# Optimization experiments

Measured on AMD Instinct MI355X. Metric: run time of the kernel, lower is better.

Reference implementation:

```python
import jax, jax.numpy as jnp
import numpy as np

B, S, H = 32, 512, 768
NHEAD, DH = 8, 96          # 8 heads * 96 = 768
E = 4096                   # edges per sample
NC = 2
NEG = -1e9
EPS = 1e-5


def _p(k, shape, scale=0.02):
    return scale * jax.random.normal(k, shape, dtype=jnp.float32)


def setup_inputs() -> dict:
    key = jax.random.key(0)
    ks = jax.random.split(key, 24)
    z = lambda *s: jnp.zeros(s, jnp.float32)
    return {
        "diff_encoded": jax.random.normal(ks[0], (B, S, H), jnp.float32),
        "msg_encoded": jax.random.normal(ks[1], (B, S, H), jnp.float32),
        "msg_mask": jnp.ones((B, S), jnp.int32),
        "edge_index_diff": jax.random.randint(ks[2], (B, 2, E), 0, S),
        "edge_index_msg": jax.random.randint(ks[3], (B, 2, E), 0, S),
        # GATv2Conv(heads=1): lin_l (source/message), lin_r (target), att vector, output bias
        "gat_wl": _p(ks[4], (H, H)), "gat_bl": z(H),
        "gat_wr": _p(ks[5], (H, H)), "gat_br": z(H),
        "gat_att": _p(ks[6], (H,)), "gat_bias": z(H),
        # cross MultiheadAttention
        "wq": _p(ks[7], (H, H)), "bq": z(H),
        "wk": _p(ks[8], (H, H)), "bk": z(H),
        "wv": _p(ks[9], (H, H)), "bv": z(H),
        "wo": _p(ks[10], (H, H)), "bo": z(H),
        # LayerNorm + MLP head
        "ln_g": jnp.ones((H,), jnp.float32), "ln_b": z(H),
        "fc0_w": _p(ks[11], (H, 512)), "fc0_b": z(512),
        "fc1_w": _p(ks[12], (512, 128)), "fc1_b": z(128),
        "fc2_w": _p(ks[13], (128, NC)), "fc2_b": z(NC),
    }


def _gat_single(x, edges, wl, bl, wr, br, att, bias):
    # GATv2Conv, heads=1, add_self_loops=True. x: [N,H], edges: [2,E] (src, dst).
    N = x.shape[0]
    src, dst = edges[0], edges[1]
    valid = (src < N) & (dst < N)            # clip_edge_index, as a mask
    src = jnp.where(valid, src, 0)
    dst = jnp.where(valid, dst, 0)
    loop = jnp.arange(N, dtype=src.dtype)    # PyG adds self loops
    src_a = jnp.concatenate([src, loop])
    dst_a = jnp.concatenate([dst, loop])
    valid_a = jnp.concatenate([valid, jnp.ones((N,), bool)])
    xl = x @ wl + bl                          # source / message transform
    xr = x @ wr + br                          # target transform
    e = jax.nn.leaky_relu(xl[src_a] + xr[dst_a], 0.2) @ att   # [E+N]
    e = jnp.where(valid_a, e, NEG)
    emax = jax.ops.segment_max(e, dst_a, num_segments=N)
    p = jnp.exp(e - emax[dst_a]) * valid_a.astype(x.dtype)
    denom = jax.ops.segment_sum(p, dst_a, num_segments=N)
    alpha = p / denom[dst_a]
    out = jax.ops.segment_sum(alpha[:, None] * xl[src_a], dst_a, num_segments=N)
    return out + bias


_gat = jax.vmap(_gat_single, in_axes=(0, 0) + (None,) * 6)


def _layernorm(x, g, b):
    mu = jnp.mean(x, -1, keepdims=True)
    var = jnp.mean(jnp.square(x - mu), -1, keepdims=True)
    return (x - mu) * jax.lax.rsqrt(var + EPS) * g + b


def reference(diff_encoded, msg_encoded, msg_mask, edge_index_diff, edge_index_msg,
              gat_wl, gat_bl, gat_wr, gat_br, gat_att, gat_bias,
              wq, bq, wk, bk, wv, bv, wo, bo, ln_g, ln_b,
              fc0_w, fc0_b, fc1_w, fc1_b, fc2_w, fc2_b):
    diff_g = _gat(diff_encoded, edge_index_diff, gat_wl, gat_bl, gat_wr, gat_br, gat_att, gat_bias) + diff_encoded
    msg_g = _gat(msg_encoded, edge_index_msg, gat_wl, gat_bl, gat_wr, gat_br, gat_att, gat_bias) + msg_encoded
    # cross attention: query=diff_g, key/value=msg_g, key_padding_mask = (msg_mask == 0)
    q = (diff_g @ wq + bq).reshape(B, S, NHEAD, DH)
    k = (msg_g @ wk + bk).reshape(B, S, NHEAD, DH)
    v = (msg_g @ wv + bv).reshape(B, S, NHEAD, DH)
    scores = jnp.einsum("bqhd,bkhd->bhqk", q, k) / jnp.sqrt(jnp.float32(DH))
    scores = jnp.where((msg_mask == 0)[:, None, None, :], NEG, scores)
    attn = jax.nn.softmax(scores, axis=-1)
    ctx = jnp.einsum("bhqk,bkhd->bqhd", attn, v).reshape(B, S, H) @ wo + bo
    fused = _layernorm(ctx + diff_g, ln_g, ln_b)
    x = fused[:, 0, :]                                  # CLS token
    x = jax.nn.relu(x @ fc0_w + fc0_b)                  # dropout = identity (eval)
    x = jax.nn.relu(x @ fc1_w + fc1_b)
    return x @ fc2_w + fc2_b
```

## Files before the change

kernel.cpp:

```cpp
#include <hip/hip_runtime.h>
#include <hip/hip_bf16.h>
#include <math.h>

#define BB 32
#define SS 512
#define HH 768
#define NHEADC 8
#define DHC 96
#define EE 4096
#define NCC 2
#define CAPC 128
#define CAP2 32
#define GSL 36
#define XRS 1536
#define NEGV -1000000000.0f
#define EPSV 1e-5f

typedef __hip_bfloat16 bf16;
typedef __bf16 bf16x8 __attribute__((ext_vector_type(8)));
typedef float f32x4 __attribute__((ext_vector_type(4)));

static __device__ inline unsigned short f2bf_u(float f) {
  __hip_bfloat16 h = __float2bfloat16(f);
  return *(unsigned short*)&h;
}
static __device__ inline float bfu(unsigned short u) {
  return __uint_as_float(((unsigned int)u) << 16);
}
static __device__ inline float bf2f(bf16 h) { return __bfloat162float(h); }

static __device__ inline void gload16(const void* g, void* l) {
  __builtin_amdgcn_global_load_lds(
      (const __attribute__((address_space(1))) void*)g,
      (__attribute__((address_space(3))) void*)l, 16, 0, 0);
}

__global__ __launch_bounds__(256) void k_cvt_bf16(const float* __restrict__ x,
                                                  bf16* __restrict__ y, int n) {
  int i = (blockIdx.x * 256 + threadIdx.x) * 4;
  if (i >= n) return;
  float4 v = *(const float4*)(x + i);
  ushort4 o;
  o.x = f2bf_u(v.x); o.y = f2bf_u(v.y); o.z = f2bf_u(v.z); o.w = f2bf_u(v.w);
  *(ushort4*)((unsigned short*)y + i) = o;
}

__global__ __launch_bounds__(256) void k_cvt_wt(
    const float* __restrict__ w0, const float* __restrict__ w1,
    const float* __restrict__ w2, const float* __restrict__ w3,
    bf16* __restrict__ o0, bf16* __restrict__ o1,
    bf16* __restrict__ o2, bf16* __restrict__ o3) {
  const float* w; bf16* o;
  switch (blockIdx.z) {
    case 0: w = w0; o = o0; break;
    case 1: w = w1; o = o1; break;
    case 2: w = w2; o = o2; break;
    default: w = w3; o = o3; break;
  }
  __shared__ float t[32][33];
  int n0 = blockIdx.x * 32, k0 = blockIdx.y * 32;
  int x = threadIdx.x & 31, y = threadIdx.x >> 5;
  for (int yy = y; yy < 32; yy += 8)
    t[yy][x] = w[(size_t)(k0 + yy) * HH + n0 + x];
  __syncthreads();
  for (int yy = y; yy < 32; yy += 8)
    o[(size_t)(n0 + yy) * HH + k0 + x] = __float2bfloat16(t[x][yy]);
}

__global__ __launch_bounds__(256) void k_bias_stack(
    const float* __restrict__ bl, const float* __restrict__ br,
    const float* __restrict__ bk, const float* __restrict__ bv,
    float* __restrict__ biasA, float* __restrict__ biasB) {
  int t = blockIdx.x * 256 + threadIdx.x;
  if (t < HH) {
    biasA[t] = bl[t]; biasA[HH + t] = br[t];
    biasB[t] = bk[t]; biasB[HH + t] = bv[t];
  }
}

template <typename OT>
__global__ __launch_bounds__(256) void k_gemm(
    const bf16* __restrict__ A, const bf16* __restrict__ Bt,
    const float* __restrict__ bias, OT* __restrict__ C,
    int M, int N, int K, int ldc)
{
  __shared__ __align__(16) bf16 As[128 * 32];
  __shared__ __align__(16) bf16 Bs[128 * 32];
  const int tid = threadIdx.x;
  const int wv = tid >> 6, lane = tid & 63;
  const int bm = blockIdx.x * 128, bn = blockIdx.y * 128;
  const int wm = (wv & 1) * 64, wn = (wv >> 1) * 64;
  const int m16 = lane & 15, half = lane >> 4;
  f32x4 acc[4][4];
  #pragma unroll
  for (int i = 0; i < 4; ++i)
    #pragma unroll
    for (int j = 0; j < 4; ++j) acc[i][j] = (f32x4){0.f, 0.f, 0.f, 0.f};

  const int c0 = tid, c1 = tid + 256;
  const int r0 = c0 >> 2, o0 = (c0 & 3) * 8;
  const int r1 = c1 >> 2, o1 = (c1 & 3) * 8;
  const size_t aB0 = (size_t)(bm + r0) * K + o0;
  const size_t aB1 = (size_t)(bm + r1) * K + o1;
  const size_t bB0 = (size_t)(bn + r0) * K + o0;
  const size_t bB1 = (size_t)(bn + r1) * K + o1;

  for (int k0 = 0; k0 < K; k0 += 32) {
    __syncthreads();
    gload16(A + aB0 + k0, As + (size_t)c0 * 8);
    gload16(A + aB1 + k0, As + (size_t)c1 * 8);
    gload16(Bt + bB0 + k0, Bs + (size_t)c0 * 8);
    gload16(Bt + bB1 + k0, Bs + (size_t)c1 * 8);
    __syncthreads();
    bf16x8 af[4], bfv[4];
    #pragma unroll
    for (int t = 0; t < 4; ++t) {
      af[t]  = *(const bf16x8*)(As + (wm + t * 16 + m16) * 32 + half * 8);
      bfv[t] = *(const bf16x8*)(Bs + (wn + t * 16 + m16) * 32 + half * 8);
    }
    #pragma unroll
    for (int i = 0; i < 4; ++i)
      #pragma unroll
      for (int j = 0; j < 4; ++j)
        acc[i][j] = __builtin_amdgcn_mfma_f32_16x16x32_bf16(af[i], bfv[j], acc[i][j], 0, 0, 0);
  }
  #pragma unroll
  for (int i = 0; i < 4; ++i) {
    #pragma unroll
    for (int j = 0; j < 4; ++j) {
      int col = bn + wn + j * 16 + m16;
      float bv = bias ? bias[col] : 0.f;
      #pragma unroll
      for (int r = 0; r < 4; ++r) {
        int row = bm + wm + i * 16 + half * 4 + r;
        float v = acc[i][j][r] + bv;
        if constexpr (sizeof(OT) == 2)
          C[(size_t)row * ldc + col] = (OT)__float2bfloat16(v);
        else
          C[(size_t)row * ldc + col] = v;
      }
    }
  }
}

__global__ __launch_bounds__(256) void k_count2(
    const int* __restrict__ e_msg, const int* __restrict__ e_diff,
    int* __restrict__ cnt, int* __restrict__ dcnt, int* __restrict__ dsrc)
{
  int i = blockIdx.x * blockDim.x + threadIdx.x;
  if (i >= BB * EE) return;
  int b = i / EE, j = i - b * EE;
  int s = e_msg[b * 2 * EE + j], d = e_msg[b * 2 * EE + EE + j];
  if (s >= 0 && s < SS && d >= 0 && d < SS)
    atomicAdd(&cnt[b * SS + d], 1);
  int s2 = e_diff[b * 2 * EE + j], d2 = e_diff[b * 2 * EE + EE + j];
  if (s2 >= 0 && s2 < SS && d2 == 0) {
    int pos = atomicAdd(&dcnt[b], 1);
    if (pos < CAPC) dsrc[b * CAPC + pos] = s2;
  }
  if (j == 0) {
    int pos = atomicAdd(&dcnt[b], 1);
    if (pos < CAPC) dsrc[b * CAPC + pos] = 0;
  }
}

__global__ __launch_bounds__(512) void k_scan(const int* __restrict__ cnt,
                                              int* __restrict__ offs,
                                              int* __restrict__ cursor) {
  __shared__ int tmp[SS];
  int b = blockIdx.x, t = threadIdx.x;
  int x = cnt[b * SS + t];
  tmp[t] = x;
  __syncthreads();
  for (int off = 1; off < SS; off <<= 1) {
    int u = (t >= off) ? tmp[t - off] : 0;
    __syncthreads();
    tmp[t] += u;
    __syncthreads();
  }
  int ex = tmp[t] - x;
  offs[b * SS + t] = ex;
  cursor[b * SS + t] = ex;
}

__global__ void k_scatter(const int* __restrict__ e_msg, int* __restrict__ cursor,
                          int* __restrict__ binned) {
  int i = blockIdx.x * blockDim.x + threadIdx.x;
  if (i >= BB * EE) return;
  int b = i / EE, j = i - b * EE;
  int s = e_msg[b * 2 * EE + j], d = e_msg[b * 2 * EE + EE + j];
  if (s >= 0 && s < SS && d >= 0 && d < SS) {
    int pos = atomicAdd(&cursor[b * SS + d], 1);
    binned[(size_t)b * EE + pos] = s;
  }
}

__global__ __launch_bounds__(256) void k_gat_fused(
    const int* __restrict__ binned, const int* __restrict__ offs,
    const int* __restrict__ cnt, const bf16* __restrict__ xlr,
    const float* __restrict__ att, const float* __restrict__ gbias,
    const float* __restrict__ resid, bf16* __restrict__ out)
{
  int g = blockIdx.x * 4 + (threadIdx.x >> 6);
  int lane = threadIdx.x & 63;
  int b = g / SS, d = g - b * SS;
  int base = offs[b * SS + d], n = cnt[b * SS + d];
  const int* bin = binned + (size_t)b * EE + base;
  float av[12];
  {
    const float4* a4 = (const float4*)att;
    #pragma unroll
    for (int r = 0; r < 3; ++r) {
      float4 t = a4[lane + 64 * r];
      av[4*r] = t.x; av[4*r+1] = t.y; av[4*r+2] = t.z; av[4*r+3] = t.w;
    }
  }
  float xr[12];
  {
    const ushort4* p = (const ushort4*)(xlr + ((size_t)b * SS + d) * XRS + HH);
    #pragma unroll
    for (int r = 0; r < 3; ++r) {
      ushort4 v = p[lane + 64 * r];
      xr[4*r] = bfu(v.x); xr[4*r+1] = bfu(v.y); xr[4*r+2] = bfu(v.z); xr[4*r+3] = bfu(v.w);
    }
  }
  float m = -3.0e38f, l = 0.f;
  float acc[12] = {};
  for (int i = -1; i < n; ++i) {
    int s = (i < 0) ? d : bin[i];
    float xs[12];
    const ushort4* p = (const ushort4*)(xlr + ((size_t)b * SS + s) * XRS);
    #pragma unroll
    for (int r = 0; r < 3; ++r) {
      ushort4 v = p[lane + 64 * r];
      xs[4*r] = bfu(v.x); xs[4*r+1] = bfu(v.y); xs[4*r+2] = bfu(v.z); xs[4*r+3] = bfu(v.w);
    }
    float e = 0.f;
    #pragma unroll
    for (int k = 0; k < 12; ++k) {
      float t = xs[k] + xr[k];
      t = t > 0.f ? t : 0.2f * t;
      e += t * av[k];
    }
    #pragma unroll
    for (int off = 32; off > 0; off >>= 1) e += __shfl_xor(e, off);
    float mn = fmaxf(m, e);
    float so = __expf(m - mn);
    float w  = __expf(e - mn);
    l = l * so + w;
    #pragma unroll
    for (int k = 0; k < 12; ++k) acc[k] = acc[k] * so + w * xs[k];
    m = mn;
  }
  float inv = 1.f / l;
  size_t o = ((size_t)b * SS + d) * HH;
  const float4* gb4 = (const float4*)gbias;
  const float4* rs4 = (const float4*)(resid + o);
  ushort4* out4 = (ushort4*)(out + o);
  #pragma unroll
  for (int r = 0; r < 3; ++r) {
    int c = lane + 64 * r;
    float4 gg = gb4[c], rr = rs4[c];
    ushort4 ov;
    ov.x = f2bf_u(acc[4*r+0] * inv + gg.x + rr.x);
    ov.y = f2bf_u(acc[4*r+1] * inv + gg.y + rr.y);
    ov.z = f2bf_u(acc[4*r+2] * inv + gg.z + rr.z);
    ov.w = f2bf_u(acc[4*r+3] * inv + gg.w + rr.w);
    out4[c] = ov;
  }
}

__global__ __launch_bounds__(192) void k_gather_diff(
    const int* __restrict__ dcnt, const int* __restrict__ dsrc,
    const float* __restrict__ diff_enc, bf16* __restrict__ G)
{
  int b = blockIdx.y, jj = blockIdx.x;
  int n = min(dcnt[b], CAP2);
  int t = threadIdx.x;
  size_t orow = ((size_t)b * GSL + jj) * HH;
  ushort4 o = {0, 0, 0, 0};
  if (jj < n || jj == CAP2) {
    int s = (jj == CAP2) ? 0 : dsrc[b * CAPC + jj];
    float4 v = ((const float4*)(diff_enc + ((size_t)b * SS + s) * HH))[t];
    o.x = f2bf_u(v.x); o.y = f2bf_u(v.y); o.z = f2bf_u(v.z); o.w = f2bf_u(v.w);
  }
  *(ushort4*)((unsigned short*)G + orow + t * 4) = o;
}

__global__ __launch_bounds__(256) void k_diff_gat0(
    const int* __restrict__ dcnt, const float* __restrict__ GD,
    const float* __restrict__ att, const float* __restrict__ gbias,
    const float* __restrict__ diff_enc, float* __restrict__ dg0)
{
  int b = blockIdx.x;
  int n = min(dcnt[b], CAP2);
  __shared__ float ee[CAP2];
  __shared__ float al[CAP2];
  __shared__ float xr0s[HH];
  int wave = threadIdx.x >> 6, lane = threadIdx.x & 63;
  for (int h = threadIdx.x; h < HH; h += 256)
    xr0s[h] = GD[((size_t)b * GSL + CAP2) * XRS + HH + h];
  __syncthreads();
  for (int jj = wave; jj < n; jj += 4) {
    const float* px = GD + ((size_t)b * GSL + jj) * XRS;
    float part = 0.f;
    #pragma unroll
    for (int r = 0; r < HH / 64; ++r) {
      int h = lane + 64 * r;
      float t = px[h] + xr0s[h];
      t = t > 0.f ? t : 0.2f * t;
      part += t * att[h];
    }
    #pragma unroll
    for (int off = 32; off > 0; off >>= 1) part += __shfl_xor(part, off);
    if (lane == 0) ee[jj] = part;
  }
  __syncthreads();
  if (threadIdx.x == 0) {
    float m = -3.0e38f;
    for (int i = 0; i < n; ++i) m = fmaxf(m, ee[i]);
    float ssum = 0.f;
    for (int i = 0; i < n; ++i) ssum += expf(ee[i] - m);
    float inv = 1.f / ssum;
    for (int i = 0; i < n; ++i) al[i] = expf(ee[i] - m) * inv;
  }
  __syncthreads();
  for (int h = threadIdx.x; h < HH; h += 256) {
    float acc = 0.f;
    for (int i = 0; i < n; ++i) acc += al[i] * GD[((size_t)b * GSL + i) * XRS + h];
    dg0[b * HH + h] = acc + gbias[h] + diff_enc[(size_t)b * SS * HH + h];
  }
}

__global__ __launch_bounds__(256) void k_colmat(
    const float* __restrict__ in, const float* __restrict__ w,
    const float* __restrict__ bias, const float* __restrict__ extra,
    float* __restrict__ outp, int Kd, int Nd, long in_stride, int relu)
{
  int b = blockIdx.y, n0 = blockIdx.x * 64;
  int tid = threadIdx.x, wv = tid >> 6, lane = tid & 63;
  __shared__ float xs[HH];
  __shared__ float red[4][64];
  const float* src = in + (size_t)b * in_stride;
  for (int k = tid; k < Kd; k += 256) xs[k] = src[k];
  __syncthreads();
  int h = n0 + lane;
  int kpw = Kd >> 2;
  int kb = wv * kpw;
  float acc = 0.f;
  for (int k = 0; k < kpw; k += 8) {
    #pragma unroll
    for (int u = 0; u < 8; ++u) {
      int kk = kb + k + u;
      acc += xs[kk] * w[(size_t)kk * Nd + h];
    }
  }
  red[wv][lane] = acc;
  __syncthreads();
  if (tid < 64) {
    float s = red[0][tid] + red[1][tid] + red[2][tid] + red[3][tid] + bias[n0 + tid];
    if (extra) s += extra[(size_t)b * Nd + n0 + tid];
    if (relu) s = fmaxf(s, 0.f);
    outp[(size_t)b * Nd + n0 + tid] = s;
  }
}

__global__ __launch_bounds__(256) void k_ln(
    const float* __restrict__ xin, const float* __restrict__ g,
    const float* __restrict__ bta, float* __restrict__ yout)
{
  int b = blockIdx.x, tid = threadIdx.x;
  __shared__ float red[4], redq[4];
  float v0 = xin[b * HH + tid];
  float v1 = xin[b * HH + tid + 256];
  float v2 = xin[b * HH + tid + 512];
  float sum = v0 + v1 + v2;
  float sq = v0 * v0 + v1 * v1 + v2 * v2;
  #pragma unroll
  for (int off = 32; off > 0; off >>= 1) { sum += __shfl_xor(sum, off); sq += __shfl_xor(sq, off); }
  int wv = tid >> 6, lane = tid & 63;
  if (lane == 0) { red[wv] = sum; redq[wv] = sq; }
  __syncthreads();
  sum = red[0] + red[1] + red[2] + red[3];
  sq = redq[0] + redq[1] + redq[2] + redq[3];
  float mu = sum / HH;
  float var = sq / HH - mu * mu;
  float scl = rsqrtf(var + EPSV);
  yout[b * HH + tid]       = (v0 - mu) * scl * g[tid]       + bta[tid];
  yout[b * HH + tid + 256] = (v1 - mu) * scl * g[tid + 256] + bta[tid + 256];
  yout[b * HH + tid + 512] = (v2 - mu) * scl * g[tid + 512] + bta[tid + 512];
}

__global__ __launch_bounds__(256) void k_fc12(
    const float* __restrict__ a0g, const float* __restrict__ fc1w,
    const float* __restrict__ fc1b, const float* __restrict__ fc2w,
    const float* __restrict__ fc2b, float* __restrict__ out)
{
  int b = blockIdx.x, tid = threadIdx.x;
  __shared__ float a0s[512];
  __shared__ float a1s[128];
  __shared__ float r1[2][128];
  for (int k = tid; k < 512; k += 256) a0s[k] = a0g[b * 512 + k];
  __syncthreads();
  int o = tid & 127, hf = tid >> 7;
  int kb = hf * 256;
  float acc = 0.f;
  for (int k = 0; k < 256; k += 8) {
    #pragma unroll
    for (int u = 0; u < 8; ++u) {
      int kk = kb + k + u;
      acc += a0s[kk] * fc1w[(size_t)kk * 128 + o];
    }
  }
  r1[hf][o] = acc;
  __syncthreads();
  if (tid < 128) a1s[tid] = fmaxf(r1[0][tid] + r1[1][tid] + fc1b[tid], 0.f);
  __syncthreads();
  if (tid < 128) {
    int oo = tid >> 6, l = tid & 63;
    float p = a1s[l] * fc2w[l * 2 + oo] + a1s[l + 64] * fc2w[(l + 64) * 2 + oo];
    #pragma unroll
    for (int off = 32; off > 0; off >>= 1) p += __shfl_xor(p, off);
    if (l == 0) out[b * NCC + oo] = p + fc2b[oo];
  }
}

__global__ __launch_bounds__(512) void k_attn(
    const float* __restrict__ q0, const bf16* __restrict__ kvb,
    const int* __restrict__ mask, float* __restrict__ ctx)
{
  int b = blockIdx.x / NHEADC, hd = blockIdx.x % NHEADC;
  __shared__ float qs[DHC];
  __shared__ float sc[SS];
  __shared__ float redm[8];
  __shared__ float reds[8];
  __shared__ float pr4[4][DHC];
  int tid = threadIdx.x;
  if (tid < DHC) qs[tid] = q0[b * HH + hd * DHC + tid];
  __syncthreads();
  const float scale = 0.10206207261596575f;
  {
    int s = tid;
    const int4* pk4 = (const int4*)(kvb + ((size_t)b * SS + s) * XRS + hd * DHC);
    float acc = 0.f;
    #pragma unroll
    for (int c = 0; c < 12; ++c) {
      int4 raw = pk4[c];
      const unsigned short* u = (const unsigned short*)&raw;
      #pragma unroll
      for (int j = 0; j < 8; ++j) acc += qs[c * 8 + j] * bfu(u[j]);
    }
    sc[s] = (mask[b * SS + s] != 0) ? acc * scale : NEGV;
  }
  __syncthreads();
  int wave = tid >> 6, lane = tid & 63;
  float m = sc[tid];
  #pragma unroll
  for (int off = 32; off > 0; off >>= 1) m = fmaxf(m, __shfl_xor(m, off));
  if (lane == 0) redm[wave] = m;
  __syncthreads();
  m = redm[0];
  #pragma unroll
  for (int i = 1; i < 8; ++i) m = fmaxf(m, redm[i]);
  float p0 = expf(sc[tid] - m);
  float ssum = p0;
  #pragma unroll
  for (int off = 32; off > 0; off >>= 1) ssum += __shfl_xor(ssum, off);
  if (lane == 0) reds[wave] = ssum;
  __syncthreads();
  ssum = reds[0] + reds[1] + reds[2] + reds[3] + reds[4] + reds[5] + reds[6] + reds[7];
  float inv = 1.f / ssum;
  sc[tid] = p0 * inv;
  __syncthreads();
  {
    int hs = tid >> 7, d = tid & 127;
    if (d < DHC) {
      const bf16* pv = kvb + ((size_t)b * SS + hs * 128) * XRS + HH + hd * DHC + d;
      float acc = 0.f;
      for (int s = 0; s < 128; s += 8) {
        #pragma unroll
        for (int u = 0; u < 8; ++u)
          acc += sc[hs * 128 + s + u] * bf2f(pv[(size_t)(s + u) * XRS]);
      }
      pr4[hs][d] = acc;
    }
  }
  __syncthreads();
  if (tid < DHC)
    ctx[b * HH + hd * DHC + tid] = pr4[0][tid] + pr4[1][tid] + pr4[2][tid] + pr4[3][tid];
}

extern "C" void kernel_launch(void* const* d_in, const int* in_sizes, int n_in,
                              void* d_out, int out_size, void* d_ws, size_t ws_size,
                              hipStream_t stream) {
  const float* diff_enc = (const float*)d_in[0];
  const float* msg_enc  = (const float*)d_in[1];
  const int*   msg_mask = (const int*)d_in[2];
  const int*   e_diff   = (const int*)d_in[3];
  const int*   e_msg    = (const int*)d_in[4];
  const float* gat_wl   = (const float*)d_in[5];
  const float* gat_bl   = (const float*)d_in[6];
  const float* gat_wr   = (const float*)d_in[7];
  const float* gat_br   = (const float*)d_in[8];
  const float* gat_att  = (const float*)d_in[9];
  const float* gat_bias = (const float*)d_in[10];
  const float* wq = (const float*)d_in[11];
  const float* bq = (const float*)d_in[12];
  const float* wk = (const float*)d_in[13];
  const float* bk = (const float*)d_in[14];
  const float* wv = (const float*)d_in[15];
  const float* bv = (const float*)d_in[16];
  const float* wo = (const float*)d_in[17];
  const float* bo = (const float*)d_in[18];
  const float* ln_g = (const float*)d_in[19];
  const float* ln_b = (const float*)d_in[20];
  const float* fc0w = (const float*)d_in[21];
  const float* fc0b = (const float*)d_in[22];
  const float* fc1w = (const float*)d_in[23];
  const float* fc1b = (const float*)d_in[24];
  const float* fc2w = (const float*)d_in[25];
  const float* fc2b = (const float*)d_in[26];
  float* out = (float*)d_out;

  char* ws = (char*)d_ws;
  size_t off = 0;
  auto alloc = [&](size_t bytes) -> void* {
    void* p = (void*)(ws + off);
    off += (bytes + 255) & ~(size_t)255;
    return p;
  };
  bf16* Abf    = (bf16*)alloc((size_t)BB * SS * HH * 2);
  bf16* xlr    = (bf16*)alloc((size_t)BB * SS * XRS * 2);
  bf16* kv     = (bf16*)alloc((size_t)BB * SS * XRS * 2);
  bf16* mg     = (bf16*)alloc((size_t)BB * SS * HH * 2);
  bf16* wtA    = (bf16*)alloc((size_t)2 * HH * HH * 2);
  bf16* wtB    = (bf16*)alloc((size_t)2 * HH * HH * 2);
  float* biasA = (float*)alloc((size_t)XRS * 4);
  float* biasB = (float*)alloc((size_t)XRS * 4);
  int*   cnt   = (int*)alloc((size_t)BB * SS * 4);
  int*   offs  = (int*)alloc((size_t)BB * SS * 4);
  int*   cursor= (int*)alloc((size_t)BB * SS * 4);
  int*   binned= (int*)alloc((size_t)BB * EE * 4);
  bf16*  G     = (bf16*)alloc((size_t)BB * GSL * HH * 2);
  float* GD    = (float*)alloc((size_t)BB * GSL * XRS * 4);
  int*   dcnt  = (int*)alloc((size_t)BB * 4);
  int*   dsrc  = (int*)alloc((size_t)BB * CAPC * 4);
  float* dg0   = (float*)alloc((size_t)BB * HH * 4);
  float* q0    = (float*)alloc((size_t)BB * HH * 4);
  float* ctx   = (float*)alloc((size_t)BB * HH * 4);
  float* fpre  = (float*)alloc((size_t)BB * HH * 4);
  float* fnrm  = (float*)alloc((size_t)BB * HH * 4);
  float* a0g   = (float*)alloc((size_t)BB * 512 * 4);

  hipMemsetAsync(cnt, 0, (size_t)BB * SS * 4, stream);
  hipMemsetAsync(dcnt, 0, (size_t)BB * 4, stream);

  const int nA = BB * SS * HH;
  k_cvt_bf16<<<nA / 1024, 256, 0, stream>>>(msg_enc, Abf, nA);
  dim3 wtGrid(HH / 32, HH / 32, 4);
  k_cvt_wt<<<wtGrid, 256, 0, stream>>>(gat_wl, gat_wr, wk, wv,
                                       wtA, wtA + (size_t)HH * HH,
                                       wtB, wtB + (size_t)HH * HH);
  k_bias_stack<<<3, 256, 0, stream>>>(gat_bl, gat_br, bk, bv, biasA, biasB);

  k_count2<<<(BB * EE + 255) / 256, 256, 0, stream>>>(e_msg, e_diff, cnt, dcnt, dsrc);
  k_scan<<<BB, SS, 0, stream>>>(cnt, offs, cursor);
  k_scatter<<<(BB * EE + 255) / 256, 256, 0, stream>>>(e_msg, cursor, binned);

  dim3 gBlk(256), gGridA((BB * SS) / 128, XRS / 128);
  k_gemm<bf16><<<gGridA, gBlk, 0, stream>>>(Abf, wtA, biasA, xlr,
                                            BB * SS, XRS, HH, XRS);
  k_gat_fused<<<(BB * SS) / 4, 256, 0, stream>>>(binned, offs, cnt, xlr,
                                                 gat_att, gat_bias, msg_enc, mg);
  k_gemm<bf16><<<gGridA, gBlk, 0, stream>>>(mg, wtB, biasB, kv,
                                            BB * SS, XRS, HH, XRS);
  {
    dim3 gg(GSL, BB);
    k_gather_diff<<<gg, 192, 0, stream>>>(dcnt, dsrc, diff_enc, G);
    dim3 gGridD((BB * GSL) / 128, XRS / 128);
    k_gemm<float><<<gGridD, gBlk, 0, stream>>>(G, wtA, biasA, GD,
                                               BB * GSL, XRS, HH, XRS);
  }
  k_diff_gat0<<<BB, 256, 0, stream>>>(dcnt, GD, gat_att, gat_bias, diff_enc, dg0);
  {
    dim3 g(HH / 64, BB);
    k_colmat<<<g, 256, 0, stream>>>(dg0, wq, bq, nullptr, q0, HH, HH, HH, 0);
  }
  k_attn<<<BB * NHEADC, 512, 0, stream>>>(q0, kv, msg_mask, ctx);
  {
    dim3 g(HH / 64, BB);
    k_colmat<<<g, 256, 0, stream>>>(ctx, wo, bo, dg0, fpre, HH, HH, HH, 0);
  }
  k_ln<<<BB, 256, 0, stream>>>(fpre, ln_g, ln_b, fnrm);
  {
    dim3 g(512 / 64, BB);
    k_colmat<<<g, 256, 0, stream>>>(fnrm, fc0w, fc0b, nullptr, a0g, HH, 512, HH, 1);
  }
  k_fc12<<<BB, 256, 0, stream>>>(a0g, fc1w, fc1b, fc2w, fc2b, out);
}
```

Baseline: 469.4 us.

## Merge prep kernels into one launch and deepen GEMM K-step to 64

Four independent preprocessing kernels (activation bf16 conversion, weight transpose/convert, bias stacking, edge counting) are combined into one launch that dispatches on block index, which removes launch gaps and lets the pieces overlap. The bf16 GEMM now loads two 32-wide K slices per iteration into separate LDS buffers. This halves the number of barrier pairs per K loop at the cost of doubled LDS use per block, which may reduce occupancy.

```diff
diff --git a/kernel.cpp b/kernel.cpp
--- a/kernel.cpp
+++ b/kernel.cpp
@@ -16,6 +16,12 @@
 #define NEGV -1000000000.0f
 #define EPSV 1e-5f
 
+#define PREP_CVT  12288
+#define PREP_WT   2304
+#define PREP_BIAS 3
+#define PREP_CNT  512
+#define PREP_TOT  (PREP_CVT + PREP_WT + PREP_BIAS + PREP_CNT)
+
 typedef __hip_bfloat16 bf16;
 typedef __bf16 bf16x8 __attribute__((ext_vector_type(8)));
 typedef float f32x4 __attribute__((ext_vector_type(4)));
@@ -35,46 +41,73 @@
       (__attribute__((address_space(3))) void*)l, 16, 0, 0);
 }
 
-__global__ __launch_bounds__(256) void k_cvt_bf16(const float* __restrict__ x,
-                                                  bf16* __restrict__ y, int n) {
-  int i = (blockIdx.x * 256 + threadIdx.x) * 4;
-  if (i >= n) return;
-  float4 v = *(const float4*)(x + i);
-  ushort4 o;
-  o.x = f2bf_u(v.x); o.y = f2bf_u(v.y); o.z = f2bf_u(v.z); o.w = f2bf_u(v.w);
-  *(ushort4*)((unsigned short*)y + i) = o;
-}
-
-__global__ __launch_bounds__(256) void k_cvt_wt(
-    const float* __restrict__ w0, const float* __restrict__ w1,
-    const float* __restrict__ w2, const float* __restrict__ w3,
-    bf16* __restrict__ o0, bf16* __restrict__ o1,
-    bf16* __restrict__ o2, bf16* __restrict__ o3) {
-  const float* w; bf16* o;
-  switch (blockIdx.z) {
-    case 0: w = w0; o = o0; break;
-    case 1: w = w1; o = o1; break;
-    case 2: w = w2; o = o2; break;
-    default: w = w3; o = o3; break;
-  }
-  __shared__ float t[32][33];
-  int n0 = blockIdx.x * 32, k0 = blockIdx.y * 32;
-  int x = threadIdx.x & 31, y = threadIdx.x >> 5;
-  for (int yy = y; yy < 32; yy += 8)
-    t[yy][x] = w[(size_t)(k0 + yy) * HH + n0 + x];
-  __syncthreads();
-  for (int yy = y; yy < 32; yy += 8)
-    o[(size_t)(n0 + yy) * HH + k0 + x] = __float2bfloat16(t[x][yy]);
-}
-
-__global__ __launch_bounds__(256) void k_bias_stack(
-    const float* __restrict__ bl, const float* __restrict__ br,
+__global__ __launch_bounds__(256) void k_prep(
+    const float* __restrict__ msg_enc, bf16* __restrict__ Abf,
+    const float* __restrict__ gat_wl, const float* __restrict__ gat_wr,
+    const float* __restrict__ wk, const float* __restrict__ wv,
+    bf16* __restrict__ wtA, bf16* __restrict__ wtB,
+    const float* __restrict__ gat_bl, const float* __restrict__ gat_br,
     const float* __restrict__ bk, const float* __restrict__ bv,
-    float* __restrict__ biasA, float* __restrict__ biasB) {
-  int t = blockIdx.x * 256 + threadIdx.x;
-  if (t < HH) {
-    biasA[t] = bl[t]; biasA[HH + t] = br[t];
-    biasB[t] = bk[t]; biasB[HH + t] = bv[t];
+    float* __restrict__ biasA, float* __restrict__ biasB,
+    const int* __restrict__ e_msg, const int* __restrict__ e_diff,
+    int* __restrict__ cnt, int* __restrict__ dcnt, int* __restrict__ dsrc)
+{
+  int blk = blockIdx.x, tid = threadIdx.x;
+  if (blk < PREP_CVT) {
+    int i = (blk * 256 + tid) * 4;
+    float4 v = *(const float4*)(msg_enc + i);
+    ushort4 o;
+    o.x = f2bf_u(v.x); o.y = f2bf_u(v.y); o.z = f2bf_u(v.z); o.w = f2bf_u(v.w);
+    *(ushort4*)((unsigned short*)Abf + i) = o;
+    return;
+  }
+  blk -= PREP_CVT;
+  if (blk < PREP_WT) {
+    int z = blk / 576, rr = blk - z * 576;
+    int bx = rr % 24, by = rr / 24;
+    const float* w; bf16* o;
+    switch (z) {
+      case 0: w = gat_wl; o = wtA; break;
+      case 1: w = gat_wr; o = wtA + (size_t)HH * HH; break;
+      case 2: w = wk;     o = wtB; break;
+      default: w = wv;    o = wtB + (size_t)HH * HH; break;
+    }
+    __shared__ float t[32][33];
+    int n0 = bx * 32, k0 = by * 32;
+    int x = tid & 31, y = tid >> 5;
+    for (int yy = y; yy < 32; yy += 8)
+      t[yy][x] = w[(size_t)(k0 + yy) * HH + n0 + x];
+    __syncthreads();
+    for (int yy = y; yy < 32; yy += 8)
+      o[(size_t)(n0 + yy) * HH + k0 + x] = __float2bfloat16(t[x][yy]);
+    return;
+  }
+  blk -= PREP_WT;
+  if (blk < PREP_BIAS) {
+    int t = blk * 256 + tid;
+    if (t < HH) {
+      biasA[t] = gat_bl[t]; biasA[HH + t] = gat_br[t];
+      biasB[t] = bk[t];     biasB[HH + t] = bv[t];
+    }
+    return;
+  }
+  blk -= PREP_BIAS;
+  {
+    int i = blk * 256 + tid;
+    if (i >= BB * EE) return;
+    int b = i / EE, j = i - b * EE;
+    int s = e_msg[b * 2 * EE + j], d = e_msg[b * 2 * EE + EE + j];
+    if (s >= 0 && s < SS && d >= 0 && d < SS)
+      atomicAdd(&cnt[b * SS + d], 1);
+    int s2 = e_diff[b * 2 * EE + j], d2 = e_diff[b * 2 * EE + EE + j];
+    if (s2 >= 0 && s2 < SS && d2 == 0) {
+      int pos = atomicAdd(&dcnt[b], 1);
+      if (pos < CAPC) dsrc[b * CAPC + pos] = s2;
+    }
+    if (j == 0) {
+      int pos = atomicAdd(&dcnt[b], 1);
+      if (pos < CAPC) dsrc[b * CAPC + pos] = 0;
+    }
   }
 }
 
@@ -84,8 +117,10 @@
     const float* __restrict__ bias, OT* __restrict__ C,
     int M, int N, int K, int ldc)
 {
-  __shared__ __align__(16) bf16 As[128 * 32];
-  __shared__ __align__(16) bf16 Bs[128 * 32];
+  __shared__ __align__(16) bf16 As0[128 * 32];
+  __shared__ __align__(16) bf16 As1[128 * 32];
+  __shared__ __align__(16) bf16 Bs0[128 * 32];
+  __shared__ __align__(16) bf16 Bs1[128 * 32];
   const int tid = threadIdx.x;
   const int wv = tid >> 6, lane = tid & 63;
   const int bm = blockIdx.x * 128, bn = blockIdx.y * 128;
@@ -105,24 +140,33 @@
   const size_t bB0 = (size_t)(bn + r0) * K + o0;
   const size_t bB1 = (size_t)(bn + r1) * K + o1;
 
-  for (int k0 = 0; k0 < K; k0 += 32) {
+  for (int k0 = 0; k0 < K; k0 += 64) {
     __syncthreads();
-    gload16(A + aB0 + k0, As + (size_t)c0 * 8);
-    gload16(A + aB1 + k0, As + (size_t)c1 * 8);
-    gload16(Bt + bB0 + k0, Bs + (size_t)c0 * 8);
-    gload16(Bt + bB1 + k0, Bs + (size_t)c1 * 8);
+    gload16(A + aB0 + k0, As0 + (size_t)c0 * 8);
+    gload16(A + aB1 + k0, As0 + (size_t)c1 * 8);
+    gload16(A + aB0 + k0 + 32, As1 + (size_t)c0 * 8);
+    gload16(A + aB1 + k0 + 32, As1 + (size_t)c1 * 8);
+    gload16(Bt + bB0 + k0, Bs0 + (size_t)c0 * 8);
+    gload16(Bt + bB1 + k0, Bs0 + (size_t)c1 * 8);
+    gload16(Bt + bB0 + k0 + 32, Bs1 + (size_t)c0 * 8);
+    gload16(Bt + bB1 + k0 + 32, Bs1 + (size_t)c1 * 8);
     __syncthreads();
-    bf16x8 af[4], bfv[4];
-    #pragma unroll
-    for (int t = 0; t < 4; ++t) {
-      af[t]  = *(const bf16x8*)(As + (wm + t * 16 + m16) * 32 + half * 8);
-      bfv[t] = *(const bf16x8*)(Bs + (wn + t * 16 + m16) * 32 + half * 8);
-    }
-    #pragma unroll
-    for (int i = 0; i < 4; ++i)
+    #pragma unroll
+    for (int ks = 0; ks < 2; ++ks) {
+      const bf16* Ah = ks ? As1 : As0;
+      const bf16* Bh = ks ? Bs1 : Bs0;
+      bf16x8 af[4], bfv[4];
       #pragma unroll
-      for (int j = 0; j < 4; ++j)
-        acc[i][j] = __builtin_amdgcn_mfma_f32_16x16x32_bf16(af[i], bfv[j], acc[i][j], 0, 0, 0);
+      for (int t = 0; t < 4; ++t) {
+        af[t]  = *(const bf16x8*)(Ah + (wm + t * 16 + m16) * 32 + half * 8);
+        bfv[t] = *(const bf16x8*)(Bh + (wn + t * 16 + m16) * 32 + half * 8);
+      }
+      #pragma unroll
+      for (int i = 0; i < 4; ++i)
+        #pragma unroll
+        for (int j = 0; j < 4; ++j)
+          acc[i][j] = __builtin_amdgcn_mfma_f32_16x16x32_bf16(af[i], bfv[j], acc[i][j], 0, 0, 0);
+    }
   }
   #pragma unroll
   for (int i = 0; i < 4; ++i) {
@@ -140,27 +184,6 @@
           C[(size_t)row * ldc + col] = v;
       }
     }
-  }
-}
-
-__global__ __launch_bounds__(256) void k_count2(
-    const int* __restrict__ e_msg, const int* __restrict__ e_diff,
-    int* __restrict__ cnt, int* __restrict__ dcnt, int* __restrict__ dsrc)
-{
-  int i = blockIdx.x * blockDim.x + threadIdx.x;
-  if (i >= BB * EE) return;
-  int b = i / EE, j = i - b * EE;
-  int s = e_msg[b * 2 * EE + j], d = e_msg[b * 2 * EE + EE + j];
-  if (s >= 0 && s < SS && d >= 0 && d < SS)
-    atomicAdd(&cnt[b * SS + d], 1);
-  int s2 = e_diff[b * 2 * EE + j], d2 = e_diff[b * 2 * EE + EE + j];
-  if (s2 >= 0 && s2 < SS && d2 == 0) {
-    int pos = atomicAdd(&dcnt[b], 1);
-    if (pos < CAPC) dsrc[b * CAPC + pos] = s2;
-  }
-  if (j == 0) {
-    int pos = atomicAdd(&dcnt[b], 1);
-    if (pos < CAPC) dsrc[b * CAPC + pos] = 0;
   }
 }
 
@@ -555,15 +578,10 @@
   hipMemsetAsync(cnt, 0, (size_t)BB * SS * 4, stream);
   hipMemsetAsync(dcnt, 0, (size_t)BB * 4, stream);
 
-  const int nA = BB * SS * HH;
-  k_cvt_bf16<<<nA / 1024, 256, 0, stream>>>(msg_enc, Abf, nA);
-  dim3 wtGrid(HH / 32, HH / 32, 4);
-  k_cvt_wt<<<wtGrid, 256, 0, stream>>>(gat_wl, gat_wr, wk, wv,
-                                       wtA, wtA + (size_t)HH * HH,
-                                       wtB, wtB + (size_t)HH * HH);
-  k_bias_stack<<<3, 256, 0, stream>>>(gat_bl, gat_br, bk, bv, biasA, biasB);
-
-  k_count2<<<(BB * EE + 255) / 256, 256, 0, stream>>>(e_msg, e_diff, cnt, dcnt, dsrc);
+  k_prep<<<PREP_TOT, 256, 0, stream>>>(msg_enc, Abf, gat_wl, gat_wr, wk, wv,
+                                       wtA, wtB, gat_bl, gat_br, bk, bv,
+                                       biasA, biasB, e_msg, e_diff,
+                                       cnt, dcnt, dsrc);
   k_scan<<<BB, SS, 0, stream>>>(cnt, offs, cursor);
   k_scatter<<<(BB * EE + 255) / 256, 256, 0, stream>>>(e_msg, cursor, binned);
 
```

Result: faster. 447.7 us (-4.6%).
